# Performance work log

Measured on AMD Instinct MI355X. Metric: run time of the kernel, lower is better.

The kernel has to match this reference:

```python
import jax, jax.numpy as jnp
import numpy as np

NEG_SLOPE = 0.2  # PyG GATConv default


def gat_layer(x, src, dst, W, a_src, a_dst, b, heads, ch, num_nodes):
    # x: [N, F_in]; W: [F_in, heads*ch]; a_src/a_dst: [heads, ch]; b: [heads*ch]
    h = (x @ W).reshape(num_nodes, heads, ch)                      # [N,H,C]
    al_s = jnp.einsum('nhc,hc->nh', h, a_src)                      # [N,H]
    al_d = jnp.einsum('nhc,hc->nh', h, a_dst)                      # [N,H]
    e = jax.nn.leaky_relu(al_s[src] + al_d[dst], NEG_SLOPE)        # [E,H]
    # segment softmax over incoming edges of each destination node
    emax = jax.ops.segment_max(e, dst, num_segments=num_nodes)     # [N,H]
    ee = jnp.exp(e - emax[dst])
    denom = jax.ops.segment_sum(ee, dst, num_segments=num_nodes)   # [N,H]
    alpha = ee / denom[dst]                                        # [E,H]
    msg = h[src] * alpha[..., None]                                # [E,H,C]
    out = jax.ops.segment_sum(msg, dst, num_segments=num_nodes)    # [N,H,C]
    return out.reshape(num_nodes, heads * ch) + b


def setup_inputs() -> dict:
    key = jax.random.key(0)
    ks = jax.random.split(key, 12)
    N, F_in, H1, C1, OUT = 50000, 128, 6, 32, 2
    E = 800000
    x = jax.random.normal(ks[0], (N, F_in), dtype=jnp.float32)
    edge_index = jax.random.randint(ks[1], (2, E), 0, N, dtype=jnp.int64)
    s = 0.1
    return {
        'x': x,
        'edge_index': edge_index,
        'W1': jax.random.normal(ks[2], (F_in, H1 * C1), dtype=jnp.float32) * s,
        'a1_src': jax.random.normal(ks[3], (H1, C1), dtype=jnp.float32) * s,
        'a1_dst': jax.random.normal(ks[4], (H1, C1), dtype=jnp.float32) * s,
        'b1': jnp.zeros((H1 * C1,), dtype=jnp.float32),
        'W2': jax.random.normal(ks[5], (H1 * C1, 1 * OUT), dtype=jnp.float32) * s,
        'a2_src': jax.random.normal(ks[6], (1, OUT), dtype=jnp.float32) * s,
        'a2_dst': jax.random.normal(ks[7], (1, OUT), dtype=jnp.float32) * s,
        'b2': jnp.zeros((OUT,), dtype=jnp.float32),
    }


def reference(x, edge_index, W1, a1_src, a1_dst, b1, W2, a2_src, a2_dst, b2):
    N = x.shape[0]
    loop = jnp.arange(N, dtype=edge_index.dtype)
    src = jnp.concatenate([edge_index[0], loop])  # add_self_loops=True (PyG default)
    dst = jnp.concatenate([edge_index[1], loop])
    h = gat_layer(x, src, dst, W1, a1_src, a1_dst, b1, heads=6, ch=32, num_nodes=N)
    h = jax.nn.relu(h)
    h = gat_layer(h, src, dst, W2, a2_src, a2_dst, b2, heads=1, ch=2, num_nodes=N)
    return jax.nn.log_softmax(h, axis=1)
```

## Files before the change

### kernel.cpp

```cpp
#include <hip/hip_runtime.h>
#include <hip/hip_fp16.h>

#define LRELU(v) ((v) > 0.0f ? (v) : 0.2f * (v))

constexpr int F_IN = 128;
constexpr int NH1  = 6;
constexpr int D1   = 192;

typedef _Float16 half8 __attribute__((ext_vector_type(8)));
typedef float floatx4 __attribute__((ext_vector_type(4)));

__device__ __forceinline__ void wave_lds_fence() {
  __builtin_amdgcn_wave_barrier();
  asm volatile("s_waitcnt lgkmcnt(0)" ::: "memory");
  __builtin_amdgcn_wave_barrier();
}

__global__ __launch_bounds__(256) void k_prep(const float* __restrict__ W1,
                                              __half* __restrict__ w1t,
                                              int* __restrict__ cnt, int N) {
  int tid = blockIdx.x * 256 + threadIdx.x;
  int nthr = gridDim.x * 256;
  for (int i = tid; i < F_IN * D1; i += nthr) {
    int k = i / D1, n = i - k * D1;
    w1t[(size_t)n * F_IN + k] = __float2half(W1[i]);
  }
  for (int i = tid; i < N; i += nthr) cnt[i] = 0;
}

__global__ __launch_bounds__(256) void k_gemm1(const float* __restrict__ x,
                                               const __half* __restrict__ w1t,
                                               const float* __restrict__ a1s,
                                               const float* __restrict__ a1d,
                                               __half* __restrict__ h1h,
                                               float* __restrict__ als,
                                               float* __restrict__ ald, int N) {
  int wv = blockIdx.x * 4 + (threadIdx.x >> 6);
  int m0 = wv * 16;
  if (m0 >= N) return;
  int lane = threadIdx.x & 63;
  int ln15 = lane & 15, q = lane >> 4;

  float avs[12], avd[12];
#pragma unroll
  for (int f = 0; f < 12; ++f) {
    int idx = (f >> 1) * 32 + (f & 1) * 16 + ln15;
    avs[f] = a1s[idx];
    avd[f] = a1d[idx];
  }

  floatx4 acc[12];
#pragma unroll
  for (int f = 0; f < 12; ++f) acc[f] = (floatx4){0.f, 0.f, 0.f, 0.f};

  int arowi = m0 + ln15;
  if (arowi >= N) arowi = N - 1;
  const float* arow = x + (size_t)arowi * F_IN + q * 8;
#pragma unroll
  for (int kc = 0; kc < F_IN; kc += 32) {
    float4 u0 = *(const float4*)(arow + kc);
    float4 u1 = *(const float4*)(arow + kc + 4);
    half8 a;
    a[0] = (_Float16)u0.x; a[1] = (_Float16)u0.y; a[2] = (_Float16)u0.z; a[3] = (_Float16)u0.w;
    a[4] = (_Float16)u1.x; a[5] = (_Float16)u1.y; a[6] = (_Float16)u1.z; a[7] = (_Float16)u1.w;
#pragma unroll
    for (int f = 0; f < 12; ++f) {
      half8 b = *(const half8*)(w1t + (size_t)(16 * f + ln15) * F_IN + kc + q * 8);
      acc[f] = __builtin_amdgcn_mfma_f32_16x16x32_f16(a, b, acc[f], 0, 0, 0);
    }
  }

#pragma unroll
  for (int f = 0; f < 12; ++f) {
#pragma unroll
    for (int r = 0; r < 4; ++r) {
      int n = m0 + q * 4 + r;
      if (n < N) h1h[(size_t)n * D1 + 16 * f + ln15] = __float2half(acc[f][r]);
    }
  }

#pragma unroll
  for (int r = 0; r < 4; ++r) {
    float ps[6] = {0.f, 0.f, 0.f, 0.f, 0.f, 0.f};
    float pd[6] = {0.f, 0.f, 0.f, 0.f, 0.f, 0.f};
#pragma unroll
    for (int f = 0; f < 12; ++f) {
      ps[f >> 1] = fmaf(acc[f][r], avs[f], ps[f >> 1]);
      pd[f >> 1] = fmaf(acc[f][r], avd[f], pd[f >> 1]);
    }
#pragma unroll
    for (int h = 0; h < 6; ++h) {
#pragma unroll
      for (int m = 8; m; m >>= 1) {
        ps[h] += __shfl_xor(ps[h], m);
        pd[h] += __shfl_xor(pd[h], m);
      }
    }
    float os = 0.f, od = 0.f;
#pragma unroll
    for (int h = 0; h < 6; ++h)
      if (ln15 == h) { os = ps[h]; od = pd[h]; }
    int n = m0 + q * 4 + r;
    if (ln15 < 6 && n < N) {
      als[(size_t)n * 6 + ln15] = os;
      ald[(size_t)n * 6 + ln15] = od;
    }
  }
}

__global__ void k_hist(const int* __restrict__ dst, int* __restrict__ cnt, int E) {
  int e = blockIdx.x * 256 + threadIdx.x;
  if (e < E) atomicAdd(&cnt[dst[e]], 1);
}

__global__ void k_scan1(const int* __restrict__ cnt, int* __restrict__ offs,
                        int* __restrict__ bsum, int N) {
  int t = threadIdx.x;
  int idx = blockIdx.x * 256 + t;
  int lane = t & 63, w = t >> 6;
  int v = (idx < N) ? cnt[idx] : 0;
  int incl = v;
#pragma unroll
  for (int d = 1; d < 64; d <<= 1) {
    int u = __shfl_up(incl, d);
    if (lane >= d) incl += u;
  }
  __shared__ int wt[4];
  if (lane == 63) wt[w] = incl;
  __syncthreads();
  int woff = 0;
  for (int i = 0; i < w; ++i) woff += wt[i];
  if (idx < N) offs[idx] = woff + incl - v;
  if (t == 255) bsum[blockIdx.x] = woff + incl;
}

__global__ void k_scan2(int* __restrict__ bsum, int* __restrict__ boff, int NB) {
  int t = threadIdx.x;
  int lane = t & 63, w = t >> 6;
  int v = (t < NB) ? bsum[t] : 0;
  int incl = v;
#pragma unroll
  for (int d = 1; d < 64; d <<= 1) {
    int u = __shfl_up(incl, d);
    if (lane >= d) incl += u;
  }
  __shared__ int wt[4];
  if (lane == 63) wt[w] = incl;
  __syncthreads();
  int woff = 0;
  for (int i = 0; i < w; ++i) woff += wt[i];
  if (t < NB) boff[t] = woff + incl - v;
}

__global__ void k_scan3(int* __restrict__ offs, int* __restrict__ cursor,
                        const int* __restrict__ boff, const int* __restrict__ bsum,
                        int N, int NB) {
  int idx = blockIdx.x * 256 + threadIdx.x;
  if (idx < N) {
    int v = offs[idx] + boff[blockIdx.x];
    offs[idx] = v;
    cursor[idx] = v;
  }
  if (idx == 0) offs[N] = boff[NB - 1] + bsum[NB - 1];
}

__global__ void k_scatter(const int* __restrict__ src, const int* __restrict__ dst,
                          int* __restrict__ cursor, int* __restrict__ ss, int E) {
  int e = blockIdx.x * 256 + threadIdx.x;
  if (e < E) {
    int d = dst[e];
    int p = atomicAdd(&cursor[d], 1);
    ss[p] = src[e];
  }
}

__global__ __launch_bounds__(256) void k_agg1(
    const __half* __restrict__ h1h, const float* __restrict__ als, const float* __restrict__ ald,
    const int* __restrict__ offs, const int* __restrict__ srcs,
    const float* __restrict__ b1, const float* __restrict__ W2,
    const float* __restrict__ a2s, const float* __restrict__ a2d,
    float* __restrict__ h2, float* __restrict__ al2s, float* __restrict__ al2d, int N) {
  __shared__ float wbuf[4][64][9];
  int wid = threadIdx.x >> 6, lane = threadIdx.x & 63;
  int d = blockIdx.x * 4 + wid;
  if (d >= N) return;
  int off = offs[d], cnt = offs[d + 1] - off;
  int tot = cnt + 1;

  float aldh[6];
  {
    const float* ap = ald + (size_t)d * 6;
    float2 q0 = *(const float2*)ap, q1 = *(const float2*)(ap + 2), q2 = *(const float2*)(ap + 4);
    aldh[0] = q0.x; aldh[1] = q0.y; aldh[2] = q1.x;
    aldh[3] = q1.y; aldh[4] = q2.x; aldh[5] = q2.y;
  }

  float dh[6] = {0.f, 0.f, 0.f, 0.f, 0.f, 0.f};
  int nchunk = (tot + 63) >> 6;

  float a0 = 0.f, a1 = 0.f, a2 = 0.f;
  const int hw = lane >> 4;
  const int hh = 4 + (lane >> 5);

  auto body = [&](int j) {
    float w_a = wbuf[wid][j][hw];
    float w_b = wbuf[wid][j][hh];
    int s = __float_as_int(wbuf[wid][j][6]);
    const __half* hp = h1h + (size_t)s * D1;
    float2 v = __half22float2(*(const __half2*)(hp + 2 * lane));
    float vh = __half2float(hp[128 + lane]);
    a0 = fmaf(w_a, v.x, a0);
    a1 = fmaf(w_a, v.y, a1);
    a2 = fmaf(w_b, vh, a2);
  };
  auto jloop = [&](int jmax) {
    int j = 0;
    for (; j + 3 < jmax; j += 4) { body(j); body(j + 1); body(j + 2); body(j + 3); }
    for (; j < jmax; ++j) body(j);
  };

  if (nchunk == 1) {
    float wreg[6];
    int sreg = 0;
    if (lane < tot) {
      int s = (lane == cnt) ? d : srcs[off + lane];
      sreg = s;
      const float* ap = als + (size_t)s * 6;
      float2 p0 = *(const float2*)ap, p1 = *(const float2*)(ap + 2), p2 = *(const float2*)(ap + 4);
      float ev[6] = {p0.x, p0.y, p1.x, p1.y, p2.x, p2.y};
#pragma unroll
      for (int h = 0; h < 6; ++h) {
        float e = ev[h] + aldh[h];
        e = LRELU(e);
        wreg[h] = __expf(e);
        dh[h] = wreg[h];
      }
    }
#pragma unroll
    for (int h = 0; h < 6; ++h) {
#pragma unroll
      for (int m = 32; m; m >>= 1) dh[h] += __shfl_xor(dh[h], m);
      dh[h] = 1.0f / dh[h];
    }
    if (lane < tot) {
#pragma unroll
      for (int h = 0; h < 6; ++h) wbuf[wid][lane][h] = wreg[h] * dh[h];
      wbuf[wid][lane][6] = __int_as_float(sreg);
    }
    wave_lds_fence();
    jloop(tot);
  } else {
    for (int c = 0; c < nchunk; ++c) {
      int i = c * 64 + lane;
      if (i < tot) {
        int s = (i == cnt) ? d : srcs[off + i];
        const float* ap = als + (size_t)s * 6;
        float2 p0 = *(const float2*)ap, p1 = *(const float2*)(ap + 2), p2 = *(const float2*)(ap + 4);
        float ev[6] = {p0.x, p0.y, p1.x, p1.y, p2.x, p2.y};
#pragma unroll
        for (int h = 0; h < 6; ++h) {
          float e = ev[h] + aldh[h];
          e = LRELU(e);
          dh[h] += __expf(e);
        }
      }
    }
#pragma unroll
    for (int h = 0; h < 6; ++h) {
#pragma unroll
      for (int m = 32; m; m >>= 1) dh[h] += __shfl_xor(dh[h], m);
      dh[h] = 1.0f / dh[h];
    }
    for (int c = 0; c < nchunk; ++c) {
      int i = c * 64 + lane;
      if (i < tot) {
        int s = (i == cnt) ? d : srcs[off + i];
        const float* ap = als + (size_t)s * 6;
        float2 p0 = *(const float2*)ap, p1 = *(const float2*)(ap + 2), p2 = *(const float2*)(ap + 4);
        float ev[6] = {p0.x, p0.y, p1.x, p1.y, p2.x, p2.y};
#pragma unroll
        for (int h = 0; h < 6; ++h) {
          float e = ev[h] + aldh[h];
          e = LRELU(e);
          wbuf[wid][lane][h] = __expf(e) * dh[h];
        }
        wbuf[wid][lane][6] = __int_as_float(s);
      }
      wave_lds_fence();
      int jmax = tot - c * 64;
      if (jmax > 64) jmax = 64;
      jloop(jmax);
      wave_lds_fence();
    }
  }

  float2 bv = *(const float2*)(b1 + 2 * lane);
  float v0 = fmaxf(a0 + bv.x, 0.f);
  float v1 = fmaxf(a1 + bv.y, 0.f);
  float v2 = fmaxf(a2 + b1[128 + lane], 0.f);
  float4 ww = *(const float4*)(W2 + 4 * lane);
  float2 wh = *(const float2*)(W2 + (128 + lane) * 2);
  float s0 = v0 * ww.x + v1 * ww.z + v2 * wh.x;
  float s1 = v0 * ww.y + v1 * ww.w + v2 * wh.y;
#pragma unroll
  for (int m = 32; m; m >>= 1) {
    s0 += __shfl_xor(s0, m);
    s1 += __shfl_xor(s1, m);
  }
  if (lane == 0) {
    h2[d * 2] = s0;
    h2[d * 2 + 1] = s1;
    al2s[d] = s0 * a2s[0] + s1 * a2s[1];
    al2d[d] = s0 * a2d[0] + s1 * a2d[1];
  }
}

__global__ __launch_bounds__(256) void k_agg2(
    const float* __restrict__ h2, const float* __restrict__ al2s,
    const float* __restrict__ al2d, const int* __restrict__ offs,
    const int* __restrict__ srcs, const float* __restrict__ b2,
    float* __restrict__ out, int N) {
  int tid = blockIdx.x * 256 + threadIdx.x;
  int g = tid >> 3, r = tid & 7;
  if (g >= N) return;
  int off = offs[g], cnt = offs[g + 1] - off;
  int tot = cnt + 1;
  float ad = al2d[g];
  float den = 0.f, o0 = 0.f, o1 = 0.f;
  for (int i = r; i < tot; i += 8) {
    int s = (i == cnt) ? g : srcs[off + i];
    float e = al2s[s] + ad;
    e = LRELU(e);
    float a = __expf(e);
    float2 hv = *(const float2*)(h2 + (size_t)s * 2);
    den += a;
    o0 = fmaf(a, hv.x, o0);
    o1 = fmaf(a, hv.y, o1);
  }
#pragma unroll
  for (int m = 4; m; m >>= 1) {
    den += __shfl_xor(den, m);
    o0 += __shfl_xor(o0, m);
    o1 += __shfl_xor(o1, m);
  }
  if (r == 0) {
    float inv = 1.0f / den;
    o0 = o0 * inv + b2[0];
    o1 = o1 * inv + b2[1];
    float mm = fmaxf(o0, o1);
    float l = mm + logf(__expf(o0 - mm) + __expf(o1 - mm));
    *(float2*)(out + (size_t)g * 2) = make_float2(o0 - l, o1 - l);
  }
}

extern "C" void kernel_launch(void* const* d_in, const int* in_sizes, int n_in,
                              void* d_out, int out_size, void* d_ws, size_t ws_size,
                              hipStream_t stream) {
  const float* x   = (const float*)d_in[0];
  const int*   ei  = (const int*)d_in[1];
  const float* W1  = (const float*)d_in[2];
  const float* a1s = (const float*)d_in[3];
  const float* a1d = (const float*)d_in[4];
  const float* b1  = (const float*)d_in[5];
  const float* W2  = (const float*)d_in[6];
  const float* a2s = (const float*)d_in[7];
  const float* a2d = (const float*)d_in[8];
  const float* b2  = (const float*)d_in[9];
  float* out = (float*)d_out;

  const int N = in_sizes[0] / F_IN;
  const int E = in_sizes[1] / 2;
  const int* srcp = ei;
  const int* dstp = ei + E;

  char* w = (char*)d_ws;
  auto alloc = [&](size_t bytes) {
    char* p = w;
    w += (bytes + 255) & ~(size_t)255;
    return p;
  };
  __half* h1h   = (__half*)alloc((size_t)N * D1 * 2);
  __half* w1t   = (__half*)alloc((size_t)F_IN * D1 * 2);
  float* als    = (float*)alloc((size_t)N * NH1 * 4);
  float* ald    = (float*)alloc((size_t)N * NH1 * 4);
  float* h2     = (float*)alloc((size_t)N * 2 * 4);
  float* al2s   = (float*)alloc((size_t)N * 4);
  float* al2d   = (float*)alloc((size_t)N * 4);
  int*   cnt    = (int*)alloc((size_t)N * 4);
  int*   offs   = (int*)alloc((size_t)(N + 1) * 4);
  int*   cursor = (int*)alloc((size_t)N * 4);
  int*   bsum   = (int*)alloc(1024);
  int*   boff   = (int*)alloc(1024);
  int*   ssort  = (int*)alloc((size_t)E * 4);

  const int NB = (N + 255) / 256;

  k_prep<<<128, 256, 0, stream>>>(W1, w1t, cnt, N);

  int nwave = (N + 15) / 16;
  k_gemm1<<<(nwave + 3) / 4, 256, 0, stream>>>(x, w1t, a1s, a1d, h1h, als, ald, N);

  k_hist<<<(E + 255) / 256, 256, 0, stream>>>(dstp, cnt, E);
  k_scan1<<<NB, 256, 0, stream>>>(cnt, offs, bsum, N);
  k_scan2<<<1, 256, 0, stream>>>(bsum, boff, NB);
  k_scan3<<<NB, 256, 0, stream>>>(offs, cursor, boff, bsum, N, NB);
  k_scatter<<<(E + 255) / 256, 256, 0, stream>>>(srcp, dstp, cursor, ssort, E);

  k_agg1<<<(N + 3) / 4, 256, 0, stream>>>(h1h, als, ald, offs, ssort, b1, W2,
                                          a2s, a2d, h2, al2s, al2d, N);
  k_agg2<<<(N * 8 + 255) / 256, 256, 0, stream>>>(h2, al2s, al2d, offs, ssort, b2, out, N);
}
```

Baseline: 278.0 us.

## Record per-edge atomic slot in histogram pass and drop atomic scatter

The histogram kernel now records the value returned by each edge's atomic increment, so the later placement kernel writes sources to offs[dst]+pose without a second round of atomics. The W1 transpose/convert is folded into the histogram kernel, the count array is zeroed with a memset, and the cursor array is removed. In exchange it adds an E-sized pose array to write and read back, and the atomic slot order stays nondeterministic.

```diff
diff --git a/kernel.cpp b/kernel.cpp
--- a/kernel.cpp
+++ b/kernel.cpp
@@ -16,16 +16,19 @@
   __builtin_amdgcn_wave_barrier();
 }
 
-__global__ __launch_bounds__(256) void k_prep(const float* __restrict__ W1,
+__global__ __launch_bounds__(256) void k_hist(const float* __restrict__ W1,
                                               __half* __restrict__ w1t,
-                                              int* __restrict__ cnt, int N) {
+                                              const int* __restrict__ dst,
+                                              int* __restrict__ cnt,
+                                              int* __restrict__ pose, int E) {
   int tid = blockIdx.x * 256 + threadIdx.x;
-  int nthr = gridDim.x * 256;
-  for (int i = tid; i < F_IN * D1; i += nthr) {
-    int k = i / D1, n = i - k * D1;
-    w1t[(size_t)n * F_IN + k] = __float2half(W1[i]);
-  }
-  for (int i = tid; i < N; i += nthr) cnt[i] = 0;
+  if (tid < F_IN * D1) {
+    int k = tid / D1, n = tid - k * D1;
+    w1t[(size_t)n * F_IN + k] = __float2half(W1[tid]);
+  }
+  if (tid < E) {
+    pose[tid] = atomicAdd(&cnt[dst[tid]], 1);
+  }
 }
 
 __global__ __launch_bounds__(256) void k_gemm1(const float* __restrict__ x,
@@ -108,11 +111,6 @@
   }
 }
 
-__global__ void k_hist(const int* __restrict__ dst, int* __restrict__ cnt, int E) {
-  int e = blockIdx.x * 256 + threadIdx.x;
-  if (e < E) atomicAdd(&cnt[dst[e]], 1);
-}
-
 __global__ void k_scan1(const int* __restrict__ cnt, int* __restrict__ offs,
                         int* __restrict__ bsum, int N) {
   int t = threadIdx.x;
@@ -152,25 +150,21 @@
   if (t < NB) boff[t] = woff + incl - v;
 }
 
-__global__ void k_scan3(int* __restrict__ offs, int* __restrict__ cursor,
-                        const int* __restrict__ boff, const int* __restrict__ bsum,
-                        int N, int NB) {
+__global__ void k_scan3(int* __restrict__ offs, const int* __restrict__ boff,
+                        const int* __restrict__ bsum, int N, int NB) {
   int idx = blockIdx.x * 256 + threadIdx.x;
-  if (idx < N) {
-    int v = offs[idx] + boff[blockIdx.x];
-    offs[idx] = v;
-    cursor[idx] = v;
-  }
+  if (idx < N) offs[idx] += boff[blockIdx.x];
   if (idx == 0) offs[N] = boff[NB - 1] + bsum[NB - 1];
 }
 
-__global__ void k_scatter(const int* __restrict__ src, const int* __restrict__ dst,
-                          int* __restrict__ cursor, int* __restrict__ ss, int E) {
+__global__ __launch_bounds__(256) void k_place(const int* __restrict__ src,
+                                               const int* __restrict__ dst,
+                                               const int* __restrict__ offs,
+                                               const int* __restrict__ pose,
+                                               int* __restrict__ ssort, int E) {
   int e = blockIdx.x * 256 + threadIdx.x;
   if (e < E) {
-    int d = dst[e];
-    int p = atomicAdd(&cursor[d], 1);
-    ss[p] = src[e];
+    ssort[offs[dst[e]] + pose[e]] = src[e];
   }
 }
 
@@ -388,23 +382,24 @@
   float* al2d   = (float*)alloc((size_t)N * 4);
   int*   cnt    = (int*)alloc((size_t)N * 4);
   int*   offs   = (int*)alloc((size_t)(N + 1) * 4);
-  int*   cursor = (int*)alloc((size_t)N * 4);
+  int*   pose   = (int*)alloc((size_t)E * 4);
   int*   bsum   = (int*)alloc(1024);
   int*   boff   = (int*)alloc(1024);
   int*   ssort  = (int*)alloc((size_t)E * 4);
 
   const int NB = (N + 255) / 256;
 
-  k_prep<<<128, 256, 0, stream>>>(W1, w1t, cnt, N);
+  hipMemsetAsync(cnt, 0, (size_t)N * 4, stream);
+
+  k_hist<<<(E + 255) / 256, 256, 0, stream>>>(W1, w1t, dstp, cnt, pose, E);
 
   int nwave = (N + 15) / 16;
   k_gemm1<<<(nwave + 3) / 4, 256, 0, stream>>>(x, w1t, a1s, a1d, h1h, als, ald, N);
 
-  k_hist<<<(E + 255) / 256, 256, 0, stream>>>(dstp, cnt, E);
   k_scan1<<<NB, 256, 0, stream>>>(cnt, offs, bsum, N);
   k_scan2<<<1, 256, 0, stream>>>(bsum, boff, NB);
-  k_scan3<<<NB, 256, 0, stream>>>(offs, cursor, boff, bsum, N, NB);
-  k_scatter<<<(E + 255) / 256, 256, 0, stream>>>(srcp, dstp, cursor, ssort, E);
+  k_scan3<<<NB, 256, 0, stream>>>(offs, boff, bsum, N, NB);
+  k_place<<<(E + 255) / 256, 256, 0, stream>>>(srcp, dstp, offs, pose, ssort, E);
 
   k_agg1<<<(N + 3) / 4, 256, 0, stream>>>(h1h, als, ald, offs, ssort, b1, W2,
                                           a2s, a2d, h2, al2s, al2d, N);
```

After: 238.9 us. 14.1% less time.
